# Kernel tuning notes

Measured on AMD Instinct MI355X. Metric: run time of the kernel, lower is better.

Reference implementation:

```python
import jax, jax.numpy as jnp
import numpy as np

DIM = 512
NUM_HEADS = 8
BALL_SIZE = 64
TOPK = 2
DIMENSIONALITY = 3
B = 2
N_BALLS = 1024
N_TOTAL = B * N_BALLS * BALL_SIZE


def setup_inputs() -> dict:
    key = jax.random.key(0)
    ks = jax.random.split(key, 6)
    s = 0.02
    return {
        "x": jax.random.normal(ks[0], (N_TOTAL, DIM), jnp.float32),
        "pos": jax.random.normal(ks[1], (N_TOTAL, DIMENSIONALITY), jnp.float32),
        "qkv_w": jax.random.normal(ks[2], (DIM, 3 * DIM), jnp.float32) * s,
        "qkv_b": jnp.zeros((3 * DIM,), jnp.float32),
        "proj_w": jax.random.normal(ks[3], (DIM, DIM), jnp.float32) * s,
        "proj_b": jnp.zeros((DIM,), jnp.float32),
        "pe_w": jax.random.normal(ks[4], (DIMENSIONALITY, DIM), jnp.float32) * s,
        "pe_b": jnp.zeros((DIM,), jnp.float32),
        "num_batches": B,
    }


def _forward(x, pos, qkv_w, qkv_b, proj_w, proj_b, pe_w, pe_b, num_batches):
    N, D = x.shape
    m = BALL_SIZE
    H = NUM_HEADS
    E = D // H
    b = num_batches
    n = N // (b * m)

    # relative position of leaves wrt ball center (torch.no_grad in original)
    p = pos.reshape(-1, m, pos.shape[-1])
    rel = (p - p.mean(axis=1, keepdims=True)).reshape(N, -1)
    rel = jax.lax.stop_gradient(rel)
    x = x + rel @ pe_w + pe_b

    # qkv split exactly like repeat('(b n m) (H E K) -> K b H n m E'): K innermost
    qkv = (x @ qkv_w + qkv_b).reshape(b, n, m, H, E, 3)
    q = jnp.transpose(qkv[..., 0], (0, 3, 1, 2, 4))  # [b,H,n,m,E]
    k = jnp.transpose(qkv[..., 1], (0, 3, 1, 2, 4))
    v = jnp.transpose(qkv[..., 2], (0, 3, 1, 2, 4))

    # The original's rearrange('b n H m E -> b H n m E') on an already
    # [b,H,n,m,E] tensor swaps head/ball axes; the subsequent repeat along a
    # fresh axis of size m*E followed by gather(dim=2) picks values that are
    # independent of the topk indices. Net effect (exactly reproduced here):
    #   desired_{k,v}[b, h, query, t, m2, e] = {k,v}[b, head=t, ball=h, m2, e]
    # i.e. every query of head h attends to keys/values of ball h taken from
    # the first `topk` heads, flattened in (t, m2) order.
    k_sel = jnp.transpose(k[:, :TOPK, :H], (0, 2, 1, 3, 4)).reshape(b, H, TOPK * m, E)
    v_sel = jnp.transpose(v[:, :TOPK, :H], (0, 2, 1, 3, 4)).reshape(b, H, TOPK * m, E)

    qf = q.reshape(b, H, n * m, E)
    scores = jnp.einsum('bhqe,bhke->bhqk', qf, k_sel) * (E ** -0.5)
    attn = jax.nn.softmax(scores, axis=-1)
    out = jnp.einsum('bhqk,bhke->bhqe', attn, v_sel)  # [b,H,n*m,E]
    out = jnp.transpose(out, (0, 2, 1, 3)).reshape(N, D)  # '(b nm) (H E)'
    return out @ proj_w + proj_b


def reference(x, pos, qkv_w, qkv_b, proj_w, proj_b, pe_w, pe_b, num_batches):
    return _forward(x, pos, qkv_w, qkv_b, proj_w, proj_b, pe_w, pe_b, num_batches)
```

## Files before the change

kernel.cpp:

```cpp
#include <hip/hip_runtime.h>

typedef __bf16 bf16;
typedef __bf16 bf16x8 __attribute__((ext_vector_type(8)));
typedef __bf16 bf16x4 __attribute__((ext_vector_type(4)));
typedef float  f32x4  __attribute__((ext_vector_type(4)));

__device__ __forceinline__ f32x4 mfma16(bf16x8 a, bf16x8 b, f32x4 c) {
    return __builtin_amdgcn_mfma_f32_16x16x32_bf16(a, b, c, 0, 0, 0);
}

__device__ __forceinline__ void gll16(const bf16* g, bf16* l) {
    __builtin_amdgcn_global_load_lds(
        (const __attribute__((address_space(1))) void*)g,
        (__attribute__((address_space(3))) void*)l, 16, 0, 0);
}

__global__ __launch_bounds__(256) void prep_weights(
    const float* __restrict__ qkv_w, const float* __restrict__ qkv_b,
    const float* __restrict__ proj_w,
    bf16* __restrict__ BqT, bf16* __restrict__ kvWT, bf16* __restrict__ projWT,
    float* __restrict__ bq, float* __restrict__ bkv)
{
    int i = blockIdx.x * 256 + threadIdx.x;
    if (i < 262144) {
        int c_ = i >> 9, k = i & 511;
        int c = (c_ >> 6) * 192 + (c_ & 63) * 3;
        BqT[i] = (bf16)(qkv_w[k * 1536 + c] * 0.125f);
        return;
    }
    i -= 262144;
    if (i < 131072) {
        int c2 = i >> 9, k = i & 511;
        int t = c2 >> 7, kk = (c2 >> 6) & 1, e = c2 & 63;
        int c = t * 192 + e * 3 + 1 + kk;
        kvWT[i] = (bf16)(qkv_w[k * 1536 + c]);
        return;
    }
    i -= 131072;
    if (i < 262144) {
        int c_ = i >> 9, k = i & 511;
        projWT[i] = (bf16)(proj_w[k * 512 + c_]);
        return;
    }
    i -= 262144;
    if (i < 512) {
        bq[i] = qkv_b[(i >> 6) * 192 + (i & 63) * 3] * 0.125f;
        return;
    }
    i -= 512;
    if (i < 256) {
        int t = i >> 7, kk = (i >> 6) & 1, e = i & 63;
        bkv[i] = qkv_b[t * 192 + e * 3 + 1 + kk];
    }
}

__global__ __launch_bounds__(256) void xprep(
    const float* __restrict__ x, const float* __restrict__ pos,
    const float* __restrict__ pe_w, const float* __restrict__ pe_b,
    bf16* __restrict__ xp)
{
    const int ball = blockIdx.x;
    const int tid = threadIdx.x;
    const size_t tok0 = (size_t)ball * 64;

    __shared__ float pw[1536];
    __shared__ float pb[512];
    __shared__ float pp[64][3];
    __shared__ float mean[3];

    for (int i = tid; i < 1536; i += 256) pw[i] = pe_w[i];
    for (int i = tid; i < 512; i += 256) pb[i] = pe_b[i];
    if (tid < 64) {
        pp[tid][0] = pos[(tok0 + tid) * 3 + 0];
        pp[tid][1] = pos[(tok0 + tid) * 3 + 1];
        pp[tid][2] = pos[(tok0 + tid) * 3 + 2];
    }
    __syncthreads();
    if (tid < 3) {
        float s = 0.f;
        #pragma unroll
        for (int i = 0; i < 64; ++i) s += pp[i][tid];
        mean[tid] = s * (1.0f / 64.0f);
    }
    __syncthreads();

    const float4* x4 = (const float4*)(x + tok0 * 512);
    bf16* op = xp + tok0 * 512;
    #pragma unroll 4
    for (int it = 0; it < 32; ++it) {
        int flat = it * 256 + tid;
        int row = flat >> 7;
        int c = (flat & 127) * 4;
        float4 xv = x4[flat];
        float r0 = pp[row][0] - mean[0];
        float r1 = pp[row][1] - mean[1];
        float r2 = pp[row][2] - mean[2];
        float v0 = xv.x + r0 * pw[c + 0] + r1 * pw[512 + c + 0] + r2 * pw[1024 + c + 0] + pb[c + 0];
        float v1 = xv.y + r0 * pw[c + 1] + r1 * pw[512 + c + 1] + r2 * pw[1024 + c + 1] + pb[c + 1];
        float v2 = xv.z + r0 * pw[c + 2] + r1 * pw[512 + c + 2] + r2 * pw[1024 + c + 2] + pb[c + 2];
        float v3 = xv.w + r0 * pw[c + 3] + r1 * pw[512 + c + 3] + r2 * pw[1024 + c + 3] + pb[c + 3];
        bf16x4 ov = { (bf16)v0, (bf16)v1, (bf16)v2, (bf16)v3 };
        *(bf16x4*)(op + (size_t)flat * 4) = ov;
    }
}

template<int EPI>
__global__ __launch_bounds__(256) void gemm_bt(
    const bf16* __restrict__ A, const bf16* __restrict__ Bt,
    const float* __restrict__ bias, void* __restrict__ Cv)
{
    const int bid = blockIdx.x;
    const int ct = bid & 3;
    const int rt = bid >> 2;
    const int row0 = rt * 128, col0 = ct * 128;
    const int tid = threadIdx.x;
    const int w = tid >> 6, l = tid & 63;
    const int wr = w >> 1, wc = w & 1;
    const int l15 = l & 15, lg = l >> 4;

    __shared__ __align__(16) bf16 As[128 * 64];
    __shared__ __align__(16) bf16 Bs[128 * 64];

    f32x4 acc[4][4] = {};

    int srow[4], scol[4];
    #pragma unroll
    for (int j = 0; j < 4; ++j) {
        int chunk = w * 4 + j;
        int o = chunk * 512 + l * 8;
        int r = o >> 6;
        int slot = (o & 63) >> 3;
        srow[j] = r;
        scol[j] = ((slot ^ (r & 7)) << 3);
    }

    for (int ks = 0; ks < 512; ks += 64) {
        #pragma unroll
        for (int j = 0; j < 4; ++j) {
            int chunk = w * 4 + j;
            gll16(A  + (size_t)(row0 + srow[j]) * 512 + ks + scol[j], &As[chunk * 512]);
            gll16(Bt + (size_t)(col0 + srow[j]) * 512 + ks + scol[j], &Bs[chunk * 512]);
        }
        __syncthreads();
        #pragma unroll
        for (int kk = 0; kk < 2; ++kk) {
            bf16x8 a[4], b[4];
            #pragma unroll
            for (int mi = 0; mi < 4; ++mi) {
                int r = wr * 64 + mi * 16 + l15;
                int slot = (kk * 4 + lg) ^ (r & 7);
                a[mi] = *(const bf16x8*)&As[r * 64 + slot * 8];
            }
            #pragma unroll
            for (int ni = 0; ni < 4; ++ni) {
                int r = wc * 64 + ni * 16 + l15;
                int slot = (kk * 4 + lg) ^ (r & 7);
                b[ni] = *(const bf16x8*)&Bs[r * 64 + slot * 8];
            }
            #pragma unroll
            for (int mi = 0; mi < 4; ++mi)
                #pragma unroll
                for (int ni = 0; ni < 4; ++ni)
                    acc[mi][ni] = mfma16(a[mi], b[ni], acc[mi][ni]);
        }
        __syncthreads();
    }

    #pragma unroll
    for (int mi = 0; mi < 4; ++mi) {
        #pragma unroll
        for (int ni = 0; ni < 4; ++ni) {
            int col = col0 + wc * 64 + ni * 16 + l15;
            float bv = bias[col];
            int rbase = row0 + wr * 64 + mi * 16 + lg * 4;
            #pragma unroll
            for (int r = 0; r < 4; ++r) {
                float vv = acc[mi][ni][r] + bv;
                if (EPI == 0) ((bf16*)Cv)[(size_t)(rbase + r) * 512 + col] = (bf16)vv;
                else          ((float*)Cv)[(size_t)(rbase + r) * 512 + col] = vv;
            }
        }
    }
}

__global__ __launch_bounds__(256) void kv_proj(
    const bf16* __restrict__ xp, const bf16* __restrict__ kvWT,
    const float* __restrict__ bkv, bf16* __restrict__ ksel, bf16* __restrict__ vselT)
{
    const int bid = blockIdx.x;
    const int b = bid >> 9;
    const int ball = (bid >> 6) & 7;
    const int m2 = bid & 63;
    const size_t tok = (size_t)b * 65536 + ball * 64 + m2;
    const int tid = threadIdx.x;

    __shared__ __align__(16) bf16 xrow[512];
    xrow[tid] = xp[tok * 512 + tid];
    xrow[tid + 256] = xp[tok * 512 + tid + 256];
    __syncthreads();

    float acc = 0.f;
    const bf16* wrp = kvWT + (size_t)tid * 512;
    #pragma unroll 8
    for (int k = 0; k < 512; k += 8) {
        bf16x8 wv = *(const bf16x8*)(wrp + k);
        bf16x8 xv = *(const bf16x8*)(&xrow[k]);
        #pragma unroll
        for (int j = 0; j < 8; ++j) acc += (float)xv[j] * (float)wv[j];
    }
    acc += bkv[tid];
    int t = tid >> 7, kk = (tid >> 6) & 1, e = tid & 63;
    if (kk == 0)
        ksel[((size_t)(b * 8 + ball) * 128 + t * 64 + m2) * 64 + e] = (bf16)acc;
    else
        vselT[((size_t)(b * 8 + ball) * 64 + e) * 128 + t * 64 + m2] = (bf16)acc;
}

__global__ __launch_bounds__(256) void attn_k(
    const bf16* __restrict__ q, const bf16* __restrict__ ksel,
    const bf16* __restrict__ vselT, bf16* __restrict__ attno)
{
    const int bid = blockIdx.x;
    const int qt = bid & 1023;
    const int bh = bid >> 10;
    const int b = bh >> 3;
    const int h = bh & 7;
    const int tid = threadIdx.x;
    const int w = tid >> 6;
    const int l = tid & 63;
    const int l15 = l & 15, lg = l >> 4;

    __shared__ __align__(16) bf16 Ks[128][72];
    __shared__ __align__(16) bf16 Vt[64][136];
    __shared__ __align__(16) bf16 Pl[4][16][136];

    const bf16* kg = ksel + (size_t)(b * 8 + h) * 128 * 64;
    #pragma unroll
    for (int it = 0; it < 8; ++it) {
        int i = it * 256 + tid;
        int r = i >> 4, c4 = (i & 15) * 4;
        *(bf16x4*)&Ks[r][c4] = *(const bf16x4*)(kg + r * 64 + c4);
    }
    const bf16* vg = vselT + (size_t)(b * 8 + h) * 64 * 128;
    #pragma unroll
    for (int it = 0; it < 8; ++it) {
        int i = it * 256 + tid;
        int r = i >> 5, c4 = (i & 31) * 4;
        *(bf16x4*)&Vt[r][c4] = *(const bf16x4*)(vg + r * 128 + c4);
    }

    const size_t tokq = (size_t)b * 65536 + (size_t)qt * 64 + w * 16 + l15;
    const bf16* qp = q + tokq * 512 + h * 64 + lg * 8;
    bf16x8 qa0 = *(const bf16x8*)qp;
    bf16x8 qa1 = *(const bf16x8*)(qp + 32);

    __syncthreads();

    f32x4 s[8];
    #pragma unroll
    for (int kt = 0; kt < 8; ++kt) {
        f32x4 a0 = {0.f, 0.f, 0.f, 0.f};
        a0 = mfma16(qa0, *(const bf16x8*)&Ks[kt * 16 + l15][lg * 8], a0);
        a0 = mfma16(qa1, *(const bf16x8*)&Ks[kt * 16 + l15][32 + lg * 8], a0);
        s[kt] = a0;
    }

    #pragma unroll
    for (int r = 0; r < 4; ++r) {
        float mx = s[0][r];
        #pragma unroll
        for (int kt = 1; kt < 8; ++kt) mx = fmaxf(mx, s[kt][r]);
        mx = fmaxf(mx, __shfl_xor(mx, 1));
        mx = fmaxf(mx, __shfl_xor(mx, 2));
        mx = fmaxf(mx, __shfl_xor(mx, 4));
        mx = fmaxf(mx, __shfl_xor(mx, 8));
        float sum = 0.f;
        #pragma unroll
        for (int kt = 0; kt < 8; ++kt) {
            float p = __expf(s[kt][r] - mx);
            s[kt][r] = p;
            sum += p;
        }
        sum += __shfl_xor(sum, 1);
        sum += __shfl_xor(sum, 2);
        sum += __shfl_xor(sum, 4);
        sum += __shfl_xor(sum, 8);
        float inv = 1.0f / sum;
        int prow = lg * 4 + r;
        #pragma unroll
        for (int kt = 0; kt < 8; ++kt)
            Pl[w][prow][kt * 16 + l15] = (bf16)(s[kt][r] * inv);
    }

    __syncthreads();

    f32x4 o[4] = { {0,0,0,0}, {0,0,0,0}, {0,0,0,0}, {0,0,0,0} };
    #pragma unroll
    for (int kc = 0; kc < 4; ++kc) {
        bf16x8 pa = *(const bf16x8*)&Pl[w][l15][kc * 32 + lg * 8];
        #pragma unroll
        for (int et = 0; et < 4; ++et)
            o[et] = mfma16(pa, *(const bf16x8*)&Vt[et * 16 + l15][kc * 32 + lg * 8], o[et]);
    }

    const size_t tokw = (size_t)b * 65536 + (size_t)qt * 64 + w * 16 + lg * 4;
    #pragma unroll
    for (int et = 0; et < 4; ++et)
        #pragma unroll
        for (int r = 0; r < 4; ++r)
            attno[(tokw + r) * 512 + h * 64 + et * 16 + l15] = (bf16)(o[et][r]);
}

extern "C" void kernel_launch(void* const* d_in, const int* in_sizes, int n_in,
                              void* d_out, int out_size, void* d_ws, size_t ws_size,
                              hipStream_t stream) {
    (void)in_sizes; (void)n_in; (void)out_size; (void)ws_size;
    const float* x      = (const float*)d_in[0];
    const float* pos    = (const float*)d_in[1];
    const float* qkv_w  = (const float*)d_in[2];
    const float* qkv_b  = (const float*)d_in[3];
    const float* proj_w = (const float*)d_in[4];
    const float* proj_b = (const float*)d_in[5];
    const float* pe_w   = (const float*)d_in[6];
    const float* pe_b   = (const float*)d_in[7];

    char* ws = (char*)d_ws;
    bf16*  Z     = (bf16*)(ws);
    bf16*  Q     = (bf16*)(ws + 134217728);
    bf16*  BqT   = (bf16*)(ws + 268435456);
    bf16*  PjT   = (bf16*)(ws + 268959744);
    bf16*  kvWT  = (bf16*)(ws + 269484032);
    bf16*  ksel  = (bf16*)(ws + 269746176);
    bf16*  vselT = (bf16*)(ws + 270008320);
    float* bq    = (float*)(ws + 270270464);
    float* bkv   = (float*)(ws + 270272512);

    prep_weights<<<2563, 256, 0, stream>>>(qkv_w, qkv_b, proj_w, BqT, kvWT, PjT, bq, bkv);
    xprep<<<2048, 256, 0, stream>>>(x, pos, pe_w, pe_b, Z);
    gemm_bt<0><<<4096, 256, 0, stream>>>(Z, BqT, bq, (void*)Q);
    kv_proj<<<1024, 256, 0, stream>>>(Z, kvWT, bkv, ksel, vselT);
    attn_k<<<16384, 256, 0, stream>>>(Q, ksel, vselT, Z);
    gemm_bt<1><<<4096, 256, 0, stream>>>(Z, PjT, proj_b, d_out);
}
```

Before: 512.1 us.

## Stage GEMM and attention epilogues through LDS for coalesced stores; swizzle block order

The GEMM epilogues now write accumulators into shared memory and then emit wide coalesced vector stores per row, where before each lane scattered scalar stores. The fp32 path does this in two halves so it fits the LDS buffer. The attention kernel's output likewise goes through the Pl scratch buffer before 16-byte row stores. A block-index remap groups workgroups across 8 slices, intended to improve cache locality. Together these add extra syncs and LDS traffic in exchange for better global store efficiency.

```diff
diff --git a/kernel.cpp b/kernel.cpp
--- a/kernel.cpp
+++ b/kernel.cpp
@@ -109,17 +109,19 @@
     const bf16* __restrict__ A, const bf16* __restrict__ Bt,
     const float* __restrict__ bias, void* __restrict__ Cv)
 {
-    const int bid = blockIdx.x;
-    const int ct = bid & 3;
-    const int rt = bid >> 2;
+    const int bid0 = blockIdx.x;
+    const int wg = (bid0 & 7) * 512 + (bid0 >> 3);
+    const int ct = wg & 3;
+    const int rt = wg >> 2;
     const int row0 = rt * 128, col0 = ct * 128;
     const int tid = threadIdx.x;
     const int w = tid >> 6, l = tid & 63;
     const int wr = w >> 1, wc = w & 1;
     const int l15 = l & 15, lg = l >> 4;
 
-    __shared__ __align__(16) bf16 As[128 * 64];
-    __shared__ __align__(16) bf16 Bs[128 * 64];
+    __shared__ __align__(16) bf16 Smem[16384];
+    bf16* As = Smem;
+    bf16* Bs = Smem + 8192;
 
     f32x4 acc[4][4] = {};
 
@@ -166,19 +168,52 @@
         __syncthreads();
     }
 
-    #pragma unroll
-    for (int mi = 0; mi < 4; ++mi) {
-        #pragma unroll
-        for (int ni = 0; ni < 4; ++ni) {
-            int col = col0 + wc * 64 + ni * 16 + l15;
-            float bv = bias[col];
-            int rbase = row0 + wr * 64 + mi * 16 + lg * 4;
-            #pragma unroll
-            for (int r = 0; r < 4; ++r) {
-                float vv = acc[mi][ni][r] + bv;
-                if (EPI == 0) ((bf16*)Cv)[(size_t)(rbase + r) * 512 + col] = (bf16)vv;
-                else          ((float*)Cv)[(size_t)(rbase + r) * 512 + col] = vv;
+    if (EPI == 0) {
+        #pragma unroll
+        for (int mi = 0; mi < 4; ++mi) {
+            #pragma unroll
+            for (int ni = 0; ni < 4; ++ni) {
+                int col = wc * 64 + ni * 16 + l15;
+                float bv = bias[col0 + col];
+                int r0l = wr * 64 + mi * 16 + lg * 4;
+                #pragma unroll
+                for (int r = 0; r < 4; ++r)
+                    Smem[(r0l + r) * 128 + col] = (bf16)(acc[mi][ni][r] + bv);
             }
+        }
+        __syncthreads();
+        int row = tid >> 1, half = tid & 1;
+        bf16* gp = (bf16*)Cv + (size_t)(row0 + row) * 512 + col0 + half * 64;
+        const bf16* lp = Smem + row * 128 + half * 64;
+        #pragma unroll
+        for (int j = 0; j < 8; ++j)
+            *(bf16x8*)(gp + j * 8) = *(const bf16x8*)(lp + j * 8);
+    } else {
+        float* Cf = (float*)Smem;
+        #pragma unroll
+        for (int p = 0; p < 2; ++p) {
+            if (wr == p) {
+                #pragma unroll
+                for (int mi = 0; mi < 4; ++mi) {
+                    #pragma unroll
+                    for (int ni = 0; ni < 4; ++ni) {
+                        int col = wc * 64 + ni * 16 + l15;
+                        float bv = bias[col0 + col];
+                        int lr0 = mi * 16 + lg * 4;
+                        #pragma unroll
+                        for (int r = 0; r < 4; ++r)
+                            Cf[(lr0 + r) * 128 + col] = acc[mi][ni][r] + bv;
+                    }
+                }
+            }
+            __syncthreads();
+            int row = tid >> 2, chunk = tid & 3;
+            float* gp = (float*)Cv + (size_t)(row0 + p * 64 + row) * 512 + col0 + chunk * 32;
+            const float* lp = Cf + row * 128 + chunk * 32;
+            #pragma unroll
+            for (int j = 0; j < 8; ++j)
+                *(float4*)(gp + j * 4) = *(const float4*)(lp + j * 4);
+            if (p == 0) __syncthreads();
         }
     }
 }
@@ -303,12 +338,24 @@
             o[et] = mfma16(pa, *(const bf16x8*)&Vt[et * 16 + l15][kc * 32 + lg * 8], o[et]);
     }
 
-    const size_t tokw = (size_t)b * 65536 + (size_t)qt * 64 + w * 16 + lg * 4;
     #pragma unroll
     for (int et = 0; et < 4; ++et)
         #pragma unroll
         for (int r = 0; r < 4; ++r)
-            attno[(tokw + r) * 512 + h * 64 + et * 16 + l15] = (bf16)(o[et][r]);
+            Pl[w][lg * 4 + r][et * 16 + l15] = (bf16)(o[et][r]);
+
+    __syncthreads();
+
+    {
+        int rowg = tid >> 2;
+        int w2 = rowg >> 4, lr = rowg & 15;
+        int chunk = tid & 3;
+        const size_t tok = (size_t)b * 65536 + (size_t)qt * 64 + rowg;
+        bf16* gp = attno + tok * 512 + h * 64 + chunk * 16;
+        const bf16* lp = &Pl[w2][lr][chunk * 16];
+        *(bf16x8*)(gp + 0) = *(const bf16x8*)(lp + 0);
+        *(bf16x8*)(gp + 8) = *(const bf16x8*)(lp + 8);
+    }
 }
 
 extern "C" void kernel_launch(void* const* d_in, const int* in_sizes, int n_in,
```

Result: slower. 560.7 us (+9.5%).
